# Kernel tuning notes

Measured on AMD Instinct MI355X. Metric: run time of the kernel, lower is better.

## Reference

```python
import jax, jax.numpy as jnp
import numpy as np

B, S, E, H, DH, F = 4, 2048, 1024, 4, 256, 4096


def setup_inputs() -> dict:
    key = jax.random.key(0)
    ks = jax.random.split(key, 16)
    def w(k, shape):
        return jax.random.normal(k, shape, jnp.float32) * 0.02
    return {
        "inputs": jax.random.normal(ks[0], (B, S, E), jnp.float32),
        "context": jax.random.normal(ks[1], (B, S, E), jnp.float32),
        # self-attention (causal) per-head projections stacked over heads
        "Wk1": w(ks[2], (H, E, DH)), "bk1": jnp.zeros((H, DH), jnp.float32),
        "Wq1": w(ks[3], (H, E, DH)), "bq1": jnp.zeros((H, DH), jnp.float32),
        "Wv1": w(ks[4], (H, E, DH)), "bv1": jnp.zeros((H, DH), jnp.float32),
        "Wo1": w(ks[5], (E, E)), "bo1": jnp.zeros((E,), jnp.float32),
        # cross-attention (no mask)
        "Wk2": w(ks[6], (H, E, DH)), "bk2": jnp.zeros((H, DH), jnp.float32),
        "Wq2": w(ks[7], (H, E, DH)), "bq2": jnp.zeros((H, DH), jnp.float32),
        "Wv2": w(ks[8], (H, E, DH)), "bv2": jnp.zeros((H, DH), jnp.float32),
        "Wo2": w(ks[9], (E, E)), "bo2": jnp.zeros((E,), jnp.float32),
        "ln_g": jnp.ones((E,), jnp.float32), "ln_b": jnp.zeros((E,), jnp.float32),
        # FFN
        "W1": w(ks[10], (E, F)), "b1": jnp.zeros((F,), jnp.float32),
        "W2": w(ks[11], (F, E)), "b2": jnp.zeros((E,), jnp.float32),
    }


def _mha(kin, vin, qin, Wk, bk, Wq, bq, Wv, bv, Wo, bo, causal):
    # per-head Dense projections, batched over heads: [B,S,E] x [H,E,DH] -> [B,H,S,DH]
    K = jnp.einsum('bse,hed->bhsd', kin, Wk) + bk[None, :, None, :]
    Q = jnp.einsum('bse,hed->bhsd', qin, Wq) + bq[None, :, None, :]
    V = jnp.einsum('bse,hed->bhsd', vin, Wv) + bv[None, :, None, :]
    # NOTE: original divides by head_dim (K.get_shape()[2]), NOT sqrt(head_dim)
    scores = jnp.einsum('bhqd,bhkd->bhqk', Q, K) / K.shape[-1]
    if causal:
        sq, sk = scores.shape[-2], scores.shape[-1]
        mask = jnp.triu(jnp.full((sq, sk), -jnp.inf, scores.dtype), k=1)
        scores = scores + mask  # additive -inf strictly above the diagonal
    A = jax.nn.softmax(scores, axis=-1)
    # concat heads in order along the feature axis, then output Dense
    out = jnp.einsum('bhqk,bhkd->bqhd', A, V).reshape(qin.shape[0], qin.shape[1], -1)
    return out @ Wo + bo


def _ln(x, g, b):
    # keras LayerNormalization default epsilon = 1e-3
    m = x.mean(-1, keepdims=True)
    v = ((x - m) ** 2).mean(-1, keepdims=True)
    return (x - m) / jnp.sqrt(v + 1e-3) * g + b


def reference(inputs, context, Wk1, bk1, Wq1, bq1, Wv1, bv1, Wo1, bo1,
              Wk2, bk2, Wq2, bq2, Wv2, bv2, Wo2, bo2,
              ln_g, ln_b, W1, b1, W2, b2):
    # dropout layers are identity at inference
    a = _mha(inputs, inputs, inputs, Wk1, bk1, Wq1, bq1, Wv1, bv1, Wo1, bo1, True) + inputs
    a = _ln(a, ln_g, ln_b)
    # cross-attention: keys/values = context, queries = normalized self-attn output
    c = _mha(context, context, a, Wk2, bk2, Wq2, bq2, Wv2, bv2, Wo2, bo2, False) + a
    c = _ln(c, ln_g, ln_b)
    h = jax.nn.relu(c @ W1 + b1) @ W2 + b2 + c
    return jax.nn.relu(_ln(h, ln_g, ln_b))
```

## Files before the change

kernel.cpp:

```cpp
#include <hip/hip_runtime.h>

#define DEV __device__ __forceinline__

typedef unsigned short u16;
typedef __bf16 bf16x8 __attribute__((ext_vector_type(8)));
typedef bf16x8 __attribute__((may_alias)) bf16x8a;
typedef float f32x4 __attribute__((ext_vector_type(4)));
typedef float f32x16 __attribute__((ext_vector_type(16)));

constexpr int NB = 4, NS = 2048, NE = 1024, NH = 4, NDH = 256, NF = 4096;
constexpr int NR = NB * NS;

DEV u16 f2bf(float f) {
  unsigned u = __float_as_uint(f);
  u += 0x7fff + ((u >> 16) & 1);
  return (u16)(u >> 16);
}

DEV f32x4 mfma16(bf16x8 a, bf16x8 b, f32x4 c) {
  return __builtin_amdgcn_mfma_f32_16x16x32_bf16(a, b, c, 0, 0, 0);
}
DEV f32x16 mfma32(bf16x8 a, bf16x8 b, f32x16 c) {
  return __builtin_amdgcn_mfma_f32_32x32x16_bf16(a, b, c, 0, 0, 0);
}

DEV bf16x8 ldfrag(const u16* p) { return *(const bf16x8a*)p; }

DEV void gload_lds16(const void* g, void* l) {
  __builtin_amdgcn_global_load_lds(
      (const __attribute__((address_space(1))) void*)g,
      (__attribute__((address_space(3))) void*)l, 16, 0, 0);
}

DEV void blockbar() {
  asm volatile("" ::: "memory");
  __builtin_amdgcn_s_barrier();
  asm volatile("" ::: "memory");
}

DEV unsigned packbf(float a, float b) {
  union { __bf16 h[2]; unsigned u; } x;
  x.h[0] = (__bf16)a; x.h[1] = (__bf16)b;
  return x.u;
}

__global__ void cast_f32_bf16(const float* __restrict__ in, u16* __restrict__ out, int n4) {
  int i = blockIdx.x * 256 + threadIdx.x;
  if (i >= n4) return;
  float4 v = ((const float4*)in)[i];
  ushort4 o;
  o.x = f2bf(v.x); o.y = f2bf(v.y); o.z = f2bf(v.z); o.w = f2bf(v.w);
  ((ushort4*)out)[i] = o;
}

__global__ void transpose_cast(const float* __restrict__ in, u16* __restrict__ out, int R, int C) {
  __shared__ float t[32][33];
  size_t base = (size_t)blockIdx.z * R * C;
  int c0 = blockIdx.x * 32, r0 = blockIdx.y * 32;
  int x = threadIdx.x;
  for (int yy = threadIdx.y; yy < 32; yy += 8)
    t[yy][x] = in[base + (size_t)(r0 + yy) * C + c0 + x];
  __syncthreads();
  for (int yy = threadIdx.y; yy < 32; yy += 8)
    out[base + (size_t)(c0 + yy) * R + r0 + x] = f2bf(t[x][yy]);
}

__global__ void transpose_v(const u16* __restrict__ V, int vstride, u16* __restrict__ Vt) {
  __shared__ u16 t[32][34];
  int bh = blockIdx.z, b = bh >> 2, h = bh & (NH - 1);
  int s0 = blockIdx.x * 32, d0 = blockIdx.y * 32;
  int x = threadIdx.x;
  for (int yy = threadIdx.y; yy < 32; yy += 8)
    t[yy][x] = V[(size_t)(b * NS + s0 + yy) * vstride + h * NDH + d0 + x];
  __syncthreads();
  for (int yy = threadIdx.y; yy < 32; yy += 8)
    Vt[((size_t)bh * NDH + d0 + yy) * NS + s0 + x] = t[x][yy];
}

__global__ void copy_f32(const float* __restrict__ s, float* __restrict__ d, int n) {
  int i = blockIdx.x * 256 + threadIdx.x;
  if (i < n) d[i] = s[i];
}

template<int BN, int OUTF32, int RELU>
__global__ __launch_bounds__(512, 1)
void gemm4r(const u16* __restrict__ A, const u16* __restrict__ Bt,
            const float* __restrict__ bias, const float* __restrict__ res,
            float* __restrict__ outF, u16* __restrict__ outB,
            int M, int N, int K)
{
  constexpr int NFRAG = BN / 64;
  constexpr int BREG = BN * 32;
  constexpr int SPH = 2 + (BN == 256 ? 2 : 1);
  __shared__ __align__(16) u16 smem[32768 + 4 * BREG];

  int tid = threadIdx.x, w = tid >> 6, lane = tid & 63;
  int lr = lane & 15, lk = lane >> 4;
  int wm = w >> 2, wn = w & 3;

  int flat = blockIdx.y * gridDim.x + blockIdx.x;
  int cpx = (gridDim.x * gridDim.y) >> 3;
  int swz = (flat & 7) * cpx + (flat >> 3);
  int bx = swz % gridDim.x, by = swz / gridDim.x;
  int rowBlk = by * 256, colBlk = bx * BN;

  f32x4 acc[8][NFRAG];
#pragma unroll
  for (int f = 0; f < 8; f++)
#pragma unroll
    for (int n = 0; n < NFRAG; n++) acc[f][n] = (f32x4){0.f, 0.f, 0.f, 0.f};

  const u16* gA = A + (size_t)rowBlk * K;
  const u16* gB = Bt + (size_t)colBlk * K;

  int Rl = lane >> 3, sl = lane & 7;

  auto stage = [&](int hs) {
    int reg = hs & 3;
    int k0 = hs * 32;
#pragma unroll
    for (int j = 0; j < 2; j++) {
      int Rbase = j * 64 + w * 8;
      int R = Rbase + Rl;
      int p = sl ^ (R & 7);
      int r = 2 * R + (p >> 2), g = p & 3;
      gload_lds16(gA + (size_t)r * K + k0 + g * 8,
                  &smem[reg * 8192 + Rbase * 64]);
    }
#pragma unroll
    for (int j = 0; j < (BN == 256 ? 2 : 1); j++) {
      int Rbase = j * 64 + w * 8;
      int R = Rbase + Rl;
      int p = sl ^ (R & 7);
      int r = 2 * R + (p >> 2), g = p & 3;
      gload_lds16(gB + (size_t)r * K + k0 + g * 8,
                  &smem[32768 + reg * BREG + Rbase * 64]);
    }
  };

  int NH32 = K >> 5;
  stage(0); stage(1); stage(2);

  for (int hs = 0; hs < NH32; hs++) {
    if (hs + 3 < NH32) stage(hs + 3);
    int rem = NH32 - 1 - hs;
    if (rem > 3) rem = 3;
    if (BN == 256) {
      if (rem == 3)      asm volatile("s_waitcnt vmcnt(12)" ::: "memory");
      else if (rem == 2) asm volatile("s_waitcnt vmcnt(8)" ::: "memory");
      else if (rem == 1) asm volatile("s_waitcnt vmcnt(4)" ::: "memory");
      else               asm volatile("s_waitcnt vmcnt(0)" ::: "memory");
    } else {
      if (rem == 3)      asm volatile("s_waitcnt vmcnt(9)" ::: "memory");
      else if (rem == 2) asm volatile("s_waitcnt vmcnt(6)" ::: "memory");
      else if (rem == 1) asm volatile("s_waitcnt vmcnt(3)" ::: "memory");
      else               asm volatile("s_waitcnt vmcnt(0)" ::: "memory");
    }
    blockbar();

    int reg = hs & 3;
    const u16* Ar = &smem[reg * 8192];
    const u16* Br = &smem[32768 + reg * BREG];
    bf16x8 af[8], bfr[NFRAG];
#pragma unroll
    for (int f = 0; f < 8; f++) {
      int rowA = wm * 128 + f * 16 + lr;
      af[f] = ldfrag(&Ar[(rowA >> 1) * 64 +
                         (((((rowA & 1) << 2) | lk) ^ ((rowA >> 1) & 7)) * 8)]);
    }
#pragma unroll
    for (int n = 0; n < NFRAG; n++) {
      int rowB = wn * (BN >> 2) + n * 16 + lr;
      bfr[n] = ldfrag(&Br[(rowB >> 1) * 64 +
                          (((((rowB & 1) << 2) | lk) ^ ((rowB >> 1) & 7)) * 8)]);
    }
    asm volatile("s_waitcnt lgkmcnt(0)" ::: "memory");
    blockbar();

    __builtin_amdgcn_s_setprio(1);
#pragma unroll
    for (int f = 0; f < 8; f++)
#pragma unroll
      for (int n = 0; n < NFRAG; n++)
        acc[f][n] = mfma16(af[f], bfr[n], acc[f][n]);
    __builtin_amdgcn_s_setprio(0);
  }

  int orow0 = rowBlk + wm * 128;
  int ocol0 = colBlk + wn * (BN >> 2);
#pragma unroll
  for (int n = 0; n < NFRAG; n++) {
    int c = ocol0 + n * 16 + lr;
    float bv = bias[c];
#pragma unroll
    for (int f = 0; f < 8; f++) {
      int r0 = orow0 + f * 16 + lk * 4;
#pragma unroll
      for (int j = 0; j < 4; j++) {
        float v = acc[f][n][j] + bv;
        if (OUTF32) v += res[(size_t)(r0 + j) * N + c];
        if (RELU) v = fmaxf(v, 0.f);
        if (OUTF32) outF[(size_t)(r0 + j) * N + c] = v;
        else        outB[(size_t)(r0 + j) * N + c] = f2bf(v);
      }
    }
  }
}

template<int CAUSAL>
__global__ __launch_bounds__(512, 2)
void attn8w(const u16* __restrict__ Qp, int qstride,
            const u16* __restrict__ Kp, int kstride,
            const u16* __restrict__ Vt, u16* __restrict__ O)
{
  __shared__ __align__(16) u16 smem[65536];

  int bidx = blockIdx.x;
  int bh = bidx & 15;
  int qt = CAUSAL ? (15 - (bidx >> 4)) : (bidx >> 4);
  int b = bh >> 2, h = bh & 3;
  int tid = threadIdx.x, w = tid >> 6, lane = tid & 63;
  int L = lane & 31, hi = lane >> 5;
  int g = w >> 1, ks = w & 1;

  int qbase = qt * 128 + g * 32;

  const u16* qrow = Qp + (size_t)(b * NS + qbase + L) * qstride + h * NDH;
  bf16x8 qf[16];
#pragma unroll
  for (int s = 0; s < 16; s++) qf[s] = ldfrag(qrow + s * 16 + hi * 8);

  f32x16 oacc[8];
#pragma unroll
  for (int db = 0; db < 8; db++) oacc[db] = (f32x16){};
  float m = -1e30f, l = 0.f;

  int nkt = CAUSAL ? (2 * qt + 2) : (NS / 64);
  constexpr float SC = 1.0f / NDH;

  const u16* kbase = Kp + (size_t)(b * NS) * kstride + h * NDH;
  const u16* vbase = Vt + (size_t)bh * NDH * NS;

  auto stage = [&](int kt, int buf) {
#pragma unroll
    for (int ii = 0; ii < 4; ii++) {
      int gi = w * 4 + ii;
      int krow = 2 * gi + hi;
      int kcol = L ^ (krow & 31);
      gload_lds16(kbase + (size_t)(kt * 64 + krow) * kstride + kcol * 8,
                  &smem[buf * 16384 + gi * 512]);
      int vd = gi * 8 + (lane >> 3);
      int vg = (lane & 7) ^ (vd & 7);
      gload_lds16(vbase + (size_t)vd * NS + kt * 64 + vg * 8,
                  &smem[32768 + buf * 16384 + gi * 512]);
    }
  };

  stage(0, 0);

  for (int kt = 0; kt < nkt; kt++) {
    int buf = kt & 1;
    const u16* bK = &smem[buf * 16384];
    const u16* bV = &smem[32768 + buf * 16384];
    if (kt + 1 < nkt) {
      stage(kt + 1, buf ^ 1);
      asm volatile("s_waitcnt vmcnt(8)" ::: "memory");
    } else {
      asm volatile("s_waitcnt vmcnt(0)" ::: "memory");
    }
    blockbar();

    int ksub0 = kt * 64 + ks * 32;
    bool skip = CAUSAL && (ksub0 > qbase + 31);
    if (!skip) {
      bool domask = CAUSAL && (ksub0 + 31 > qbase);
      __builtin_amdgcn_s_setprio(1);
      f32x16 sa = (f32x16){};
#pragma unroll
      for (int s = 0; s < 16; s++) {
        int row = ks * 32 + L;
        bf16x8 kf = ldfrag(&bK[row * 256 + (((2 * s + hi) ^ L) & 31) * 8]);
        sa = mfma32(kf, qf[s], sa);
      }
      __builtin_amdgcn_s_setprio(0);

      float p[16];
      float tmax = -1e30f;
#pragma unroll
      for (int r = 0; r < 16; r++) {
        float v = sa[r] * SC;
        if (domask) {
          int key = ksub0 + (r & 3) + 8 * (r >> 2) + 4 * hi;
          if (key > qbase + L) v = -1e30f;
        }
        p[r] = v;
        tmax = fmaxf(tmax, v);
      }
      tmax = fmaxf(tmax, __shfl_xor(tmax, 32));

      float mn = m;
      if (!__all(tmax - m <= 5.0f)) {
        mn = fmaxf(m, tmax);
        float rs = __expf(m - mn);
        m = mn;
        l *= rs;
#pragma unroll
        for (int db = 0; db < 8; db++)
#pragma unroll
          for (int r = 0; r < 16; r++) oacc[db][r] *= rs;
      }
      float psum = 0.f;
#pragma unroll
      for (int r = 0; r < 16; r++) {
        p[r] = __expf(p[r] - mn);
        psum += p[r];
      }
      psum += __shfl_xor(psum, 32);
      l += psum;

      unsigned pk01 = packbf(p[0], p[1]),  pk23 = packbf(p[2], p[3]);
      unsigned pk45 = packbf(p[4], p[5]),  pk67 = packbf(p[6], p[7]);
      unsigned pk89 = packbf(p[8], p[9]),  pkab = packbf(p[10], p[11]);
      unsigned pkcd = packbf(p[12], p[13]), pkef = packbf(p[14], p[15]);
      unsigned s45 = (unsigned)__shfl_xor((int)pk45, 32);
      unsigned s67 = (unsigned)__shfl_xor((int)pk67, 32);
      unsigned s01 = (unsigned)__shfl_xor((int)pk01, 32);
      unsigned s23 = (unsigned)__shfl_xor((int)pk23, 32);
      unsigned scd = (unsigned)__shfl_xor((int)pkcd, 32);
      unsigned sef = (unsigned)__shfl_xor((int)pkef, 32);
      unsigned s89 = (unsigned)__shfl_xor((int)pk89, 32);
      unsigned sab = (unsigned)__shfl_xor((int)pkab, 32);
      union { unsigned u[4]; bf16x8 v; } fb0, fb1;
      fb0.u[0] = hi ? s45 : pk01;
      fb0.u[1] = hi ? s67 : pk23;
      fb0.u[2] = hi ? pk45 : s01;
      fb0.u[3] = hi ? pk67 : s23;
      fb1.u[0] = hi ? scd : pk89;
      fb1.u[1] = hi ? sef : pkab;
      fb1.u[2] = hi ? pkcd : s89;
      fb1.u[3] = hi ? pkef : sab;
      bf16x8 pb0 = fb0.v, pb1 = fb1.v;

      __builtin_amdgcn_s_setprio(1);
#pragma unroll
      for (int db = 0; db < 8; db++) {
        int vd = db * 32 + L;
        bf16x8 vf0 = ldfrag(&bV[vd * 64 + (((ks * 4 + hi) ^ (vd & 7)) & 7) * 8]);
        bf16x8 vf1 = ldfrag(&bV[vd * 64 + (((ks * 4 + 2 + hi) ^ (vd & 7)) & 7) * 8]);
        oacc[db] = mfma32(vf0, pb0, oacc[db]);
        oacc[db] = mfma32(vf1, pb1, oacc[db]);
      }
      __builtin_amdgcn_s_setprio(0);
    }
    blockbar();
  }

  float* fsm = (float*)smem;
  blockbar();
  if (hi == 0) { fsm[w * 64 + L * 2] = m; fsm[w * 64 + L * 2 + 1] = l; }
  blockbar();
  float mb = fsm[(w ^ 1) * 64 + L * 2];
  float lb = fsm[(w ^ 1) * 64 + L * 2 + 1];
  float M = fmaxf(m, mb);
  float eo = __expf(m - M);
  float lt = l * eo + lb * __expf(mb - M);
  blockbar();
  float* reg = fsm + g * 8192;
  if (w & 1) {
#pragma unroll
    for (int db = 0; db < 8; db++)
#pragma unroll
      for (int r = 0; r < 16; r++) {
        int d = db * 32 + (r & 3) + 8 * (r >> 2) + 4 * hi;
        reg[d * 32 + L] = oacc[db][r] * eo;
      }
  }
  blockbar();
  if (!(w & 1)) {
    float inv = 1.f / lt;
    size_t orow = (size_t)(b * NS + qbase + L) * NE + h * NDH;
#pragma unroll
    for (int db = 0; db < 8; db++) {
#pragma unroll
      for (int rq = 0; rq < 4; rq++) {
        int d0 = db * 32 + rq * 8 + hi * 4;
        float a0 = (oacc[db][rq * 4 + 0] * eo + reg[(d0 + 0) * 32 + L]) * inv;
        float a1 = (oacc[db][rq * 4 + 1] * eo + reg[(d0 + 1) * 32 + L]) * inv;
        float a2 = (oacc[db][rq * 4 + 2] * eo + reg[(d0 + 2) * 32 + L]) * inv;
        float a3 = (oacc[db][rq * 4 + 3] * eo + reg[(d0 + 3) * 32 + L]) * inv;
        uint2 wv;
        wv.x = packbf(a0, a1);
        wv.y = packbf(a2, a3);
        *(uint2*)&O[orow + d0] = wv;
      }
    }
  }
}

template<int RELU, int WBF>
__global__ __launch_bounds__(256)
void ln_kernel(const float* __restrict__ x, const float* __restrict__ g,
               const float* __restrict__ bb, float* __restrict__ outF,
               u16* __restrict__ outB)
{
  int row = blockIdx.x, tid = threadIdx.x;
  float4 v = ((const float4*)(x + (size_t)row * NE))[tid];
  float s = v.x + v.y + v.z + v.w;
  float s2 = v.x * v.x + v.y * v.y + v.z * v.z + v.w * v.w;
#pragma unroll
  for (int off = 32; off; off >>= 1) {
    s += __shfl_xor(s, off);
    s2 += __shfl_xor(s2, off);
  }
  __shared__ float red[8];
  int wid = tid >> 6, lane = tid & 63;
  if (lane == 0) { red[wid] = s; red[4 + wid] = s2; }
  __syncthreads();
  s = red[0] + red[1] + red[2] + red[3];
  s2 = red[4] + red[5] + red[6] + red[7];
  float mean = s * (1.f / NE);
  float var = s2 * (1.f / NE) - mean * mean;
  float rstd = rsqrtf(var + 1e-3f);
  float4 gg = ((const float4*)g)[tid];
  float4 bv = ((const float4*)bb)[tid];
  float4 o;
  o.x = (v.x - mean) * rstd * gg.x + bv.x;
  o.y = (v.y - mean) * rstd * gg.y + bv.y;
  o.z = (v.z - mean) * rstd * gg.z + bv.z;
  o.w = (v.w - mean) * rstd * gg.w + bv.w;
  if (RELU) {
    o.x = fmaxf(o.x, 0.f); o.y = fmaxf(o.y, 0.f);
    o.z = fmaxf(o.z, 0.f); o.w = fmaxf(o.w, 0.f);
  }
  ((float4*)(outF + (size_t)row * NE))[tid] = o;
  if (WBF) {
    ushort4 ob;
    ob.x = f2bf(o.x); ob.y = f2bf(o.y); ob.z = f2bf(o.z); ob.w = f2bf(o.w);
    ((ushort4*)(outB + (size_t)row * NE))[tid] = ob;
  }
}

constexpr size_t OFF_X    = 0;
constexpr size_t OFF_W    = OFF_X + 16777216;
constexpr size_t OFF_BIAS = OFF_W + 33554432;
constexpr size_t OFF_QKV  = OFF_BIAS + 32768;
constexpr size_t OFF_VT   = OFF_QKV + 50331648;
constexpr size_t OFF_T0   = OFF_VT + 16777216;
constexpr size_t OFF_A    = OFF_T0 + 33554432;
constexpr size_t OFF_ABF  = OFF_A + 33554432;

extern "C" void kernel_launch(void* const* d_in, const int* in_sizes, int n_in,
                              void* d_out, int out_size, void* d_ws, size_t ws_size,
                              hipStream_t stream) {
  (void)in_sizes; (void)n_in; (void)out_size; (void)ws_size;
  const float* inp = (const float*)d_in[0];
  const float* ctx = (const float*)d_in[1];
  const float* Wk1 = (const float*)d_in[2];  const float* bk1 = (const float*)d_in[3];
  const float* Wq1 = (const float*)d_in[4];  const float* bq1 = (const float*)d_in[5];
  const float* Wv1 = (const float*)d_in[6];  const float* bv1 = (const float*)d_in[7];
  const float* Wo1 = (const float*)d_in[8];  const float* bo1 = (const float*)d_in[9];
  const float* Wk2 = (const float*)d_in[10]; const float* bk2 = (const float*)d_in[11];
  const float* Wq2 = (const float*)d_in[12]; const float* bq2 = (const float*)d_in[13];
  const float* Wv2 = (const float*)d_in[14]; const float* bv2 = (const float*)d_in[15];
  const float* Wo2 = (const float*)d_in[16]; const float* bo2 = (const float*)d_in[17];
  const float* lng = (const float*)d_in[18]; const float* lnb = (const float*)d_in[19];
  const float* W1  = (const float*)d_in[20]; const float* b1  = (const float*)d_in[21];
  const float* W2  = (const float*)d_in[22]; const float* b2  = (const float*)d_in[23];
  float* out = (float*)d_out;
  char* ws = (char*)d_ws;

  u16* XBF    = (u16*)(ws + OFF_X);
  u16* WQKV1T = (u16*)(ws + OFF_W);
  u16* WKV2T  = WQKV1T + 3072 * 1024;
  u16* WQ2T   = WKV2T + 2048 * 1024;
  u16* WO1T   = WQ2T + 1024 * 1024;
  u16* WO2T   = WO1T + 1024 * 1024;
  u16* W1T    = WO2T + 1024 * 1024;
  u16* W2T    = W1T + 4096 * 1024;
  float* BQKV1 = (float*)(ws + OFF_BIAS);
  float* BKV2  = BQKV1 + 3072;
  u16* QKV  = (u16*)(ws + OFF_QKV);
  u16* Q2   = QKV + 8192 * 2048;
  u16* VT   = (u16*)(ws + OFF_VT);
  u16* MID  = QKV;
  float* T0 = (float*)(ws + OFF_T0);
  float* Af = (float*)(ws + OFF_A);
  u16* ABF  = (u16*)(ws + OFF_ABF);
  u16* Obuf = XBF;

  dim3 tb(32, 8);

  cast_f32_bf16<<<8192, 256, 0, stream>>>(inp, XBF, NR * NE / 4);
  transpose_cast<<<dim3(8, 32, 4), tb, 0, stream>>>(Wk1, WQKV1T,               NE, NDH);
  transpose_cast<<<dim3(8, 32, 4), tb, 0, stream>>>(Wq1, WQKV1T + 1024 * 1024, NE, NDH);
  transpose_cast<<<dim3(8, 32, 4), tb, 0, stream>>>(Wv1, WQKV1T + 2048 * 1024, NE, NDH);
  transpose_cast<<<dim3(32, 32, 1), tb, 0, stream>>>(Wo1, WO1T, NE, NE);
  transpose_cast<<<dim3(8, 32, 4), tb, 0, stream>>>(Wk2, WKV2T,               NE, NDH);
  transpose_cast<<<dim3(8, 32, 4), tb, 0, stream>>>(Wv2, WKV2T + 1024 * 1024, NE, NDH);
  transpose_cast<<<dim3(8, 32, 4), tb, 0, stream>>>(Wq2, WQ2T, NE, NDH);
  transpose_cast<<<dim3(32, 32, 1), tb, 0, stream>>>(Wo2, WO2T, NE, NE);
  transpose_cast<<<dim3(128, 32, 1), tb, 0, stream>>>(W1, W1T, NE, NF);
  transpose_cast<<<dim3(32, 128, 1), tb, 0, stream>>>(W2, W2T, NF, NE);
  copy_f32<<<4, 256, 0, stream>>>(bk1, BQKV1, 1024);
  copy_f32<<<4, 256, 0, stream>>>(bq1, BQKV1 + 1024, 1024);
  copy_f32<<<4, 256, 0, stream>>>(bv1, BQKV1 + 2048, 1024);
  copy_f32<<<4, 256, 0, stream>>>(bk2, BKV2, 1024);
  copy_f32<<<4, 256, 0, stream>>>(bv2, BKV2 + 1024, 1024);

  gemm4r<256, 0, 0><<<dim3(12, 32), 512, 0, stream>>>(XBF, WQKV1T, BQKV1, nullptr,
                                                      nullptr, QKV, NR, 3072, NE);
  transpose_v<<<dim3(64, 8, 16), tb, 0, stream>>>(QKV + 2048, 3072, VT);
  attn8w<1><<<256, 512, 0, stream>>>(QKV + 1024, 3072, QKV, 3072, VT, Obuf);
  gemm4r<128, 1, 0><<<dim3(8, 32), 512, 0, stream>>>(Obuf, WO1T, bo1, inp,
                                                     T0, nullptr, NR, NE, NE);
  ln_kernel<0, 1><<<NR, 256, 0, stream>>>(T0, lng, lnb, Af, ABF);

  cast_f32_bf16<<<8192, 256, 0, stream>>>(ctx, XBF, NR * NE / 4);
  gemm4r<256, 0, 0><<<dim3(8, 32), 512, 0, stream>>>(XBF, WKV2T, BKV2, nullptr,
                                                     nullptr, QKV, NR, 2048, NE);
  gemm4r<128, 0, 0><<<dim3(8, 32), 512, 0, stream>>>(ABF, WQ2T, bq2, nullptr,
                                                     nullptr, Q2, NR, NE, NE);
  transpose_v<<<dim3(64, 8, 16), tb, 0, stream>>>(QKV + 1024, 2048, VT);
  attn8w<0><<<256, 512, 0, stream>>>(Q2, 1024, QKV, 2048, VT, Obuf);
  gemm4r<128, 1, 0><<<dim3(8, 32), 512, 0, stream>>>(Obuf, WO2T, bo2, Af,
                                                     T0, nullptr, NR, NE, NE);
  ln_kernel<0, 1><<<NR, 256, 0, stream>>>(T0, lng, lnb, Af, ABF);

  gemm4r<256, 0, 1><<<dim3(16, 32), 512, 0, stream>>>(ABF, W1T, b1, nullptr,
                                                      nullptr, MID, NR, NF, NE);
  gemm4r<128, 1, 0><<<dim3(8, 32), 512, 0, stream>>>(MID, W2T, b2, Af,
                                                     T0, nullptr, NR, NE, NF);
  ln_kernel<1, 0><<<NR, 256, 0, stream>>>(T0, lng, lnb, out, nullptr);
}
```

Measured before the change: 755.6 us.

## Repack K/V into fragment-major layout and load attention operands directly from global

Adds repack kernels that rewrite K and V into an MFMA-fragment-major layout. The attention kernel then uses 128-thread blocks, with each wave loading its K/V fragments straight from global/L2 into registers. This removes the LDS staging, the block barriers and the cross-wave split-K merge, and causal waves stop at their own diagonal. The cost is an extra repack pass over K plus redundant global reads, since the two waves in a block fetch the same K/V tiles with no LDS reuse and more load latency is exposed.

```diff
diff --git a/kernel.cpp b/kernel.cpp
--- a/kernel.cpp
+++ b/kernel.cpp
@@ -65,16 +65,36 @@
     out[base + (size_t)(c0 + yy) * R + r0 + x] = f2bf(t[x][yy]);
 }
 
-__global__ void transpose_v(const u16* __restrict__ V, int vstride, u16* __restrict__ Vt) {
-  __shared__ u16 t[32][34];
-  int bh = blockIdx.z, b = bh >> 2, h = bh & (NH - 1);
-  int s0 = blockIdx.x * 32, d0 = blockIdx.y * 32;
-  int x = threadIdx.x;
-  for (int yy = threadIdx.y; yy < 32; yy += 8)
-    t[yy][x] = V[(size_t)(b * NS + s0 + yy) * vstride + h * NDH + d0 + x];
+__global__ void repack_k(const u16* __restrict__ K, int kstride, u16* __restrict__ KF) {
+  __shared__ u16 t[32][40];
+  int bh = blockIdx.z, b = bh >> 2, h = bh & 3;
+  int k0 = blockIdx.x * 32, d0 = blockIdx.y * 32;
+  int x = threadIdx.x, y = threadIdx.y;
+  for (int key = y; key < 32; key += 8)
+    t[key][x] = K[(size_t)(b * NS + k0 + key) * kstride + h * NDH + d0 + x];
   __syncthreads();
-  for (int yy = threadIdx.y; yy < 32; yy += 8)
-    Vt[((size_t)bh * NDH + d0 + yy) * NS + s0 + x] = t[x][yy];
+  if (y < 4) {
+    int d8 = (d0 >> 3) + y;
+    uint4 v = *(const uint4*)&t[x][y * 8];
+    *(uint4*)&KF[(((size_t)bh * 32 + d8) * NS + k0 + x) * 8] = v;
+  }
+}
+
+__global__ void repack_v(const u16* __restrict__ V, int vstride, u16* __restrict__ VF) {
+  __shared__ u16 t[32][40];
+  int bh = blockIdx.z, b = bh >> 2, h = bh & 3;
+  int k0 = blockIdx.x * 32, d0 = blockIdx.y * 32;
+  int x = threadIdx.x, y = threadIdx.y;
+  for (int key = y; key < 32; key += 8)
+    t[key][x] = V[(size_t)(b * NS + k0 + key) * vstride + h * NDH + d0 + x];
+  __syncthreads();
+  if (y < 4) {
+    int key8 = (k0 >> 3) + y;
+    union { u16 h[8]; uint4 v; } val;
+#pragma unroll
+    for (int kk = 0; kk < 8; kk++) val.h[kk] = t[y * 8 + kk][x];
+    *(uint4*)&VF[(((size_t)bh * 256 + key8) * 256 + d0 + x) * 8] = val.v;
+  }
 }
 
 __global__ void copy_f32(const float* __restrict__ s, float* __restrict__ d, int n) {
@@ -91,7 +111,6 @@
 {
   constexpr int NFRAG = BN / 64;
   constexpr int BREG = BN * 32;
-  constexpr int SPH = 2 + (BN == 256 ? 2 : 1);
   __shared__ __align__(16) u16 smem[32768 + 4 * BREG];
 
   int tid = threadIdx.x, w = tid >> 6, lane = tid & 63;
@@ -208,191 +227,128 @@
 }
 
 template<int CAUSAL>
-__global__ __launch_bounds__(512, 2)
-void attn8w(const u16* __restrict__ Qp, int qstride,
-            const u16* __restrict__ Kp, int kstride,
-            const u16* __restrict__ Vt, u16* __restrict__ O)
+__global__ __launch_bounds__(128, 2)
+void attn_reg(const u16* __restrict__ Qp, int qstride,
+              const u16* __restrict__ KF, const u16* __restrict__ VF,
+              u16* __restrict__ O)
 {
-  __shared__ __align__(16) u16 smem[65536];
-
   int bidx = blockIdx.x;
   int bh = bidx & 15;
-  int qt = CAUSAL ? (15 - (bidx >> 4)) : (bidx >> 4);
+  int qt = CAUSAL ? (31 - (bidx >> 4)) : (bidx >> 4);
   int b = bh >> 2, h = bh & 3;
   int tid = threadIdx.x, w = tid >> 6, lane = tid & 63;
   int L = lane & 31, hi = lane >> 5;
-  int g = w >> 1, ks = w & 1;
-
-  int qbase = qt * 128 + g * 32;
+  int qbase = qt * 64 + w * 32;
 
   const u16* qrow = Qp + (size_t)(b * NS + qbase + L) * qstride + h * NDH;
   bf16x8 qf[16];
 #pragma unroll
   for (int s = 0; s < 16; s++) qf[s] = ldfrag(qrow + s * 16 + hi * 8);
 
+  const u16* kfb = KF + (size_t)bh * 32 * NS * 8;
+  const u16* vfb = VF + (size_t)bh * 256 * 256 * 8;
+
   f32x16 oacc[8];
 #pragma unroll
   for (int db = 0; db < 8; db++) oacc[db] = (f32x16){};
   float m = -1e30f, l = 0.f;
 
-  int nkt = CAUSAL ? (2 * qt + 2) : (NS / 64);
+  int nkt = CAUSAL ? (2 * qt + w + 1) : (NS / 32);
+  int kdiag = 2 * qt + w;
   constexpr float SC = 1.0f / NDH;
 
-  const u16* kbase = Kp + (size_t)(b * NS) * kstride + h * NDH;
-  const u16* vbase = Vt + (size_t)bh * NDH * NS;
-
-  auto stage = [&](int kt, int buf) {
-#pragma unroll
-    for (int ii = 0; ii < 4; ii++) {
-      int gi = w * 4 + ii;
-      int krow = 2 * gi + hi;
-      int kcol = L ^ (krow & 31);
-      gload_lds16(kbase + (size_t)(kt * 64 + krow) * kstride + kcol * 8,
-                  &smem[buf * 16384 + gi * 512]);
-      int vd = gi * 8 + (lane >> 3);
-      int vg = (lane & 7) ^ (vd & 7);
-      gload_lds16(vbase + (size_t)vd * NS + kt * 64 + vg * 8,
-                  &smem[32768 + buf * 16384 + gi * 512]);
-    }
-  };
-
-  stage(0, 0);
-
   for (int kt = 0; kt < nkt; kt++) {
-    int buf = kt & 1;
-    const u16* bK = &smem[buf * 16384];
-    const u16* bV = &smem[32768 + buf * 16384];
-    if (kt + 1 < nkt) {
-      stage(kt + 1, buf ^ 1);
-      asm volatile("s_waitcnt vmcnt(8)" ::: "memory");
-    } else {
-      asm volatile("s_waitcnt vmcnt(0)" ::: "memory");
-    }
-    blockbar();
-
-    int ksub0 = kt * 64 + ks * 32;
-    bool skip = CAUSAL && (ksub0 > qbase + 31);
-    if (!skip) {
-      bool domask = CAUSAL && (ksub0 + 31 > qbase);
-      __builtin_amdgcn_s_setprio(1);
-      f32x16 sa = (f32x16){};
-#pragma unroll
-      for (int s = 0; s < 16; s++) {
-        int row = ks * 32 + L;
-        bf16x8 kf = ldfrag(&bK[row * 256 + (((2 * s + hi) ^ L) & 31) * 8]);
-        sa = mfma32(kf, qf[s], sa);
+    f32x16 sa0 = (f32x16){}, sa1 = (f32x16){};
+    __builtin_amdgcn_s_setprio(1);
+#pragma unroll
+    for (int s = 0; s < 16; s++) {
+      bf16x8 kf = ldfrag(kfb + ((size_t)(2 * s + hi) * NS + kt * 32 + L) * 8);
+      if (s & 1) sa1 = mfma32(kf, qf[s], sa1);
+      else       sa0 = mfma32(kf, qf[s], sa0);
+    }
+    __builtin_amdgcn_s_setprio(0);
+
+    float p[16];
+    float tmax = -1e30f;
+    bool domask = CAUSAL && (kt == kdiag);
+#pragma unroll
+    for (int r = 0; r < 16; r++) {
+      float v = (sa0[r] + sa1[r]) * SC;
+      if (domask) {
+        int key = kt * 32 + (r & 3) + 8 * (r >> 2) + 4 * hi;
+        if (key > qbase + L) v = -1e30f;
       }
-      __builtin_amdgcn_s_setprio(0);
-
-      float p[16];
-      float tmax = -1e30f;
-#pragma unroll
-      for (int r = 0; r < 16; r++) {
-        float v = sa[r] * SC;
-        if (domask) {
-          int key = ksub0 + (r & 3) + 8 * (r >> 2) + 4 * hi;
-          if (key > qbase + L) v = -1e30f;
-        }
-        p[r] = v;
-        tmax = fmaxf(tmax, v);
-      }
-      tmax = fmaxf(tmax, __shfl_xor(tmax, 32));
-
-      float mn = m;
-      if (!__all(tmax - m <= 5.0f)) {
-        mn = fmaxf(m, tmax);
-        float rs = __expf(m - mn);
-        m = mn;
-        l *= rs;
-#pragma unroll
-        for (int db = 0; db < 8; db++)
-#pragma unroll
-          for (int r = 0; r < 16; r++) oacc[db][r] *= rs;
-      }
-      float psum = 0.f;
-#pragma unroll
-      for (int r = 0; r < 16; r++) {
-        p[r] = __expf(p[r] - mn);
-        psum += p[r];
-      }
-      psum += __shfl_xor(psum, 32);
-      l += psum;
-
-      unsigned pk01 = packbf(p[0], p[1]),  pk23 = packbf(p[2], p[3]);
-      unsigned pk45 = packbf(p[4], p[5]),  pk67 = packbf(p[6], p[7]);
-      unsigned pk89 = packbf(p[8], p[9]),  pkab = packbf(p[10], p[11]);
-      unsigned pkcd = packbf(p[12], p[13]), pkef = packbf(p[14], p[15]);
-      unsigned s45 = (unsigned)__shfl_xor((int)pk45, 32);
-      unsigned s67 = (unsigned)__shfl_xor((int)pk67, 32);
-      unsigned s01 = (unsigned)__shfl_xor((int)pk01, 32);
-      unsigned s23 = (unsigned)__shfl_xor((int)pk23, 32);
-      unsigned scd = (unsigned)__shfl_xor((int)pkcd, 32);
-      unsigned sef = (unsigned)__shfl_xor((int)pkef, 32);
-      unsigned s89 = (unsigned)__shfl_xor((int)pk89, 32);
-      unsigned sab = (unsigned)__shfl_xor((int)pkab, 32);
-      union { unsigned u[4]; bf16x8 v; } fb0, fb1;
-      fb0.u[0] = hi ? s45 : pk01;
-      fb0.u[1] = hi ? s67 : pk23;
-      fb0.u[2] = hi ? pk45 : s01;
-      fb0.u[3] = hi ? pk67 : s23;
-      fb1.u[0] = hi ? scd : pk89;
-      fb1.u[1] = hi ? sef : pkab;
-      fb1.u[2] = hi ? pkcd : s89;
-      fb1.u[3] = hi ? pkef : sab;
-      bf16x8 pb0 = fb0.v, pb1 = fb1.v;
-
-      __builtin_amdgcn_s_setprio(1);
-#pragma unroll
-      for (int db = 0; db < 8; db++) {
-        int vd = db * 32 + L;
-        bf16x8 vf0 = ldfrag(&bV[vd * 64 + (((ks * 4 + hi) ^ (vd & 7)) & 7) * 8]);
-        bf16x8 vf1 = ldfrag(&bV[vd * 64 + (((ks * 4 + 2 + hi) ^ (vd & 7)) & 7) * 8]);
-        oacc[db] = mfma32(vf0, pb0, oacc[db]);
-        oacc[db] = mfma32(vf1, pb1, oacc[db]);
-      }
-      __builtin_amdgcn_s_setprio(0);
-    }
-    blockbar();
-  }
-
-  float* fsm = (float*)smem;
-  blockbar();
-  if (hi == 0) { fsm[w * 64 + L * 2] = m; fsm[w * 64 + L * 2 + 1] = l; }
-  blockbar();
-  float mb = fsm[(w ^ 1) * 64 + L * 2];
-  float lb = fsm[(w ^ 1) * 64 + L * 2 + 1];
-  float M = fmaxf(m, mb);
-  float eo = __expf(m - M);
-  float lt = l * eo + lb * __expf(mb - M);
-  blockbar();
-  float* reg = fsm + g * 8192;
-  if (w & 1) {
-#pragma unroll
-    for (int db = 0; db < 8; db++)
-#pragma unroll
-      for (int r = 0; r < 16; r++) {
-        int d = db * 32 + (r & 3) + 8 * (r >> 2) + 4 * hi;
-        reg[d * 32 + L] = oacc[db][r] * eo;
-      }
-  }
-  blockbar();
-  if (!(w & 1)) {
-    float inv = 1.f / lt;
-    size_t orow = (size_t)(b * NS + qbase + L) * NE + h * NDH;
+      p[r] = v;
+      tmax = fmaxf(tmax, v);
+    }
+    tmax = fmaxf(tmax, __shfl_xor(tmax, 32));
+
+    float mn = m;
+    if (!__all(tmax - m <= 5.0f)) {
+      mn = fmaxf(m, tmax);
+      float rs = __expf(m - mn);
+      m = mn;
+      l *= rs;
+#pragma unroll
+      for (int db = 0; db < 8; db++)
+#pragma unroll
+        for (int r = 0; r < 16; r++) oacc[db][r] *= rs;
+    }
+    float psum = 0.f;
+#pragma unroll
+    for (int r = 0; r < 16; r++) {
+      p[r] = __expf(p[r] - mn);
+      psum += p[r];
+    }
+    psum += __shfl_xor(psum, 32);
+    l += psum;
+
+    unsigned pk01 = packbf(p[0], p[1]),  pk23 = packbf(p[2], p[3]);
+    unsigned pk45 = packbf(p[4], p[5]),  pk67 = packbf(p[6], p[7]);
+    unsigned pk89 = packbf(p[8], p[9]),  pkab = packbf(p[10], p[11]);
+    unsigned pkcd = packbf(p[12], p[13]), pkef = packbf(p[14], p[15]);
+    unsigned s45 = (unsigned)__shfl_xor((int)pk45, 32);
+    unsigned s67 = (unsigned)__shfl_xor((int)pk67, 32);
+    unsigned s01 = (unsigned)__shfl_xor((int)pk01, 32);
+    unsigned s23 = (unsigned)__shfl_xor((int)pk23, 32);
+    unsigned scd = (unsigned)__shfl_xor((int)pkcd, 32);
+    unsigned sef = (unsigned)__shfl_xor((int)pkef, 32);
+    unsigned s89 = (unsigned)__shfl_xor((int)pk89, 32);
+    unsigned sab = (unsigned)__shfl_xor((int)pkab, 32);
+    union { unsigned u[4]; bf16x8 v; } fb0, fb1;
+    fb0.u[0] = hi ? s45 : pk01;
+    fb0.u[1] = hi ? s67 : pk23;
+    fb0.u[2] = hi ? pk45 : s01;
+    fb0.u[3] = hi ? pk67 : s23;
+    fb1.u[0] = hi ? scd : pk89;
+    fb1.u[1] = hi ? sef : pkab;
+    fb1.u[2] = hi ? pkcd : s89;
+    fb1.u[3] = hi ? pkef : sab;
+    bf16x8 pb0 = fb0.v, pb1 = fb1.v;
+
+    __builtin_amdgcn_s_setprio(1);
 #pragma unroll
     for (int db = 0; db < 8; db++) {
-#pragma unroll
-      for (int rq = 0; rq < 4; rq++) {
-        int d0 = db * 32 + rq * 8 + hi * 4;
-        float a0 = (oacc[db][rq * 4 + 0] * eo + reg[(d0 + 0) * 32 + L]) * inv;
-        float a1 = (oacc[db][rq * 4 + 1] * eo + reg[(d0 + 1) * 32 + L]) * inv;
-        float a2 = (oacc[db][rq * 4 + 2] * eo + reg[(d0 + 2) * 32 + L]) * inv;
-        float a3 = (oacc[db][rq * 4 + 3] * eo + reg[(d0 + 3) * 32 + L]) * inv;
-        uint2 wv;
-        wv.x = packbf(a0, a1);
-        wv.y = packbf(a2, a3);
-        *(uint2*)&O[orow + d0] = wv;
-      }
+      bf16x8 vf0 = ldfrag(vfb + ((size_t)(kt * 4 + hi) * 256 + db * 32 + L) * 8);
+      bf16x8 vf1 = ldfrag(vfb + ((size_t)(kt * 4 + 2 + hi) * 256 + db * 32 + L) * 8);
+      oacc[db] = mfma32(vf0, pb0, oacc[db]);
+      oacc[db] = mfma32(vf1, pb1, oacc[db]);
+    }
+    __builtin_amdgcn_s_setprio(0);
+  }
+
+  float inv = 1.f / l;
+  size_t orow = (size_t)(b * NS + qbase + L) * NE + h * NDH;
+#pragma unroll
+  for (int db = 0; db < 8; db++) {
+#pragma unroll
+    for (int rq = 0; rq < 4; rq++) {
+      float a0 = oacc[db][rq * 4 + 0] * inv, a1 = oacc[db][rq * 4 + 1] * inv;
+      float a2 = oacc[db][rq * 4 + 2] * inv, a3 = oacc[db][rq * 4 + 3] * inv;
+      uint2 wv;
+      wv.x = packbf(a0, a1);
+      wv.y = packbf(a2, a3);
+      *(uint2*)&O[orow + db * 32 + rq * 8 + hi * 4] = wv;
     }
   }
 }
@@ -481,9 +437,10 @@
   float* BKV2  = BQKV1 + 3072;
   u16* QKV  = (u16*)(ws + OFF_QKV);
   u16* Q2   = QKV + 8192 * 2048;
-  u16* VT   = (u16*)(ws + OFF_VT);
+  u16* VF   = (u16*)(ws + OFF_VT);
   u16* MID  = QKV;
   float* T0 = (float*)(ws + OFF_T0);
+  u16* KF   = (u16*)T0;
   float* Af = (float*)(ws + OFF_A);
   u16* ABF  = (u16*)(ws + OFF_ABF);
   u16* Obuf = XBF;
@@ -509,8 +466,9 @@
 
   gemm4r<256, 0, 0><<<dim3(12, 32), 512, 0, stream>>>(XBF, WQKV1T, BQKV1, nullptr,
                                                       nullptr, QKV, NR, 3072, NE);
-  transpose_v<<<dim3(64, 8, 16), tb, 0, stream>>>(QKV + 2048, 3072, VT);
-  attn8w<1><<<256, 512, 0, stream>>>(QKV + 1024, 3072, QKV, 3072, VT, Obuf);
+  repack_k<<<dim3(64, 8, 16), tb, 0, stream>>>(QKV, 3072, KF);
+  repack_v<<<dim3(64, 8, 16), tb, 0, stream>>>(QKV + 2048, 3072, VF);
+  attn_reg<1><<<512, 128, 0, stream>>>(QKV + 1024, 3072, KF, VF, Obuf);
   gemm4r<128, 1, 0><<<dim3(8, 32), 512, 0, stream>>>(Obuf, WO1T, bo1, inp,
                                                      T0, nullptr, NR, NE, NE);
   ln_kernel<0, 1><<<NR, 256, 0, stream>>>(T0, lng, lnb, Af, ABF);
@@ -520,8 +478,9 @@
                                                      nullptr, QKV, NR, 2048, NE);
   gemm4r<128, 0, 0><<<dim3(8, 32), 512, 0, stream>>>(ABF, WQ2T, bq2, nullptr,
                                                      nullptr, Q2, NR, NE, NE);
-  transpose_v<<<dim3(64, 8, 16), tb, 0, stream>>>(QKV + 1024, 2048, VT);
-  attn8w<0><<<256, 512, 0, stream>>>(Q2, 1024, QKV, 2048, VT, Obuf);
+  repack_k<<<dim3(64, 8, 16), tb, 0, stream>>>(QKV, 2048, KF);
+  repack_v<<<dim3(64, 8, 16), tb, 0, stream>>>(QKV + 1024, 2048, VF);
+  attn_reg<0><<<512, 128, 0, stream>>>(Q2, 1024, KF, VF, Obuf);
   gemm4r<128, 1, 0><<<dim3(8, 32), 512, 0, stream>>>(Obuf, WO2T, bo2, Af,
                                                      T0, nullptr, NR, NE, NE);
   ln_kernel<0, 1><<<NR, 256, 0, stream>>>(T0, lng, lnb, Af, ABF);
```

Result: slower. 1.325 ms (+75.3%).
